# Optimization experiments

Hardware: AMD Instinct MI355X
Metric: run time of the kernel (lower is better)

Reference implementation:

```python
import jax, jax.numpy as jnp
import numpy as np

E = 2048        # embed_dim
HQ = 32         # num_query_heads
HKV = 8         # num_kv_heads
HD = E // HQ    # head_dim = 64
GROUP = HQ // HKV  # q_per_kv = 4
B, T = 2, 2048


def setup_inputs() -> dict:
    key = jax.random.key(0)
    ks = jax.random.split(key, 6)
    s = 0.02
    x  = jax.random.normal(ks[0], (B, T, E), dtype=jnp.float32)
    Wq = jax.random.normal(ks[1], (E, E), dtype=jnp.float32) * s
    Wk = jax.random.normal(ks[2], (E, HKV * HD), dtype=jnp.float32) * s
    Wv = jax.random.normal(ks[3], (E, HKV * HD), dtype=jnp.float32) * s
    Wo = jax.random.normal(ks[4], (E, E), dtype=jnp.float32) * s
    bo = jax.random.normal(ks[5], (E,), dtype=jnp.float32) * s
    return {"x": x, "Wq": Wq, "Wk": Wk, "Wv": Wv, "Wo": Wo, "bo": bo}


def reference(x, Wq, Wk, Wv, Wo, bo):
    Bc, Tc, _ = x.shape
    # projections
    q = (x @ Wq).reshape(Bc, Tc, HQ, HD).transpose(0, 2, 1, 3)      # [B,HQ,T,HD]
    k = (x @ Wk).reshape(Bc, Tc, HKV, HD).transpose(0, 2, 1, 3)     # [B,HKV,T,HD]
    v = (x @ Wv).reshape(Bc, Tc, HKV, HD).transpose(0, 2, 1, 3)     # [B,HKV,T,HD]
    # group queries by kv head instead of repeating k/v: [B,HKV,GROUP,T,HD]
    qg = q.reshape(Bc, HKV, GROUP, Tc, HD)
    scale = 1.0 / jnp.sqrt(jnp.asarray(HD, dtype=x.dtype))
    scores = jnp.einsum('bhgqd,bhkd->bhgqk', qg, k) * scale         # [B,HKV,GROUP,T,T]
    weights = jax.nn.softmax(scores, axis=-1)
    attn = jnp.einsum('bhgqk,bhkd->bhgqd', weights, v)              # [B,HKV,GROUP,T,HD]
    out = attn.reshape(Bc, HQ, Tc, HD).transpose(0, 2, 1, 3).reshape(Bc, Tc, E)
    return out @ Wo + bo
```

## Files before the change

### kernel.cpp

```cpp
#include <hip/hip_runtime.h>
#include <hip/hip_bf16.h>
#include <stdint.h>

#define E_ 2048
#define HQ_ 32
#define HKV_ 8
#define HD_ 64
#define B_ 2
#define T_ 2048
#define MROWS (B_*T_)
#define NKV (HKV_*HD_)
#define NQKV (E_ + 2*NKV)
#define SCALE_LOG2E 0.18033688011112042f

typedef __bf16 bf16_t;
typedef __bf16 bf16x8 __attribute__((ext_vector_type(8)));
typedef float f32x4 __attribute__((ext_vector_type(4)));

typedef const __attribute__((address_space(1))) unsigned int glb_u32;
typedef __attribute__((address_space(3))) unsigned int lds_u32;

__device__ __forceinline__ unsigned short f2bf_bits(float f) {
  unsigned int u = __float_as_uint(f);
  u += 0x7FFFu + ((u >> 16) & 1u);
  return (unsigned short)(u >> 16);
}
__device__ __forceinline__ bf16_t f2bf(float f) {
  union { unsigned short s; bf16_t h; } u;
  u.s = f2bf_bits(f);
  return u.h;
}

__global__ void cast_x_kernel(const float* __restrict__ in, bf16_t* __restrict__ out, int n8) {
  int i = blockIdx.x * blockDim.x + threadIdx.x;
  int stride = gridDim.x * blockDim.x;
  for (; i < n8; i += stride) {
    const float4* p = reinterpret_cast<const float4*>(in) + (size_t)i * 2;
    float4 a = p[0], b = p[1];
    union { unsigned short s[8]; uint4 v; } u;
    u.s[0] = f2bf_bits(a.x); u.s[1] = f2bf_bits(a.y);
    u.s[2] = f2bf_bits(a.z); u.s[3] = f2bf_bits(a.w);
    u.s[4] = f2bf_bits(b.x); u.s[5] = f2bf_bits(b.y);
    u.s[6] = f2bf_bits(b.z); u.s[7] = f2bf_bits(b.w);
    reinterpret_cast<uint4*>(out)[i] = u.v;
  }
}

__global__ void transpose_cast_w(const float* __restrict__ in, bf16_t* __restrict__ out,
                                 int R, int C) {
  __shared__ float tile[32][33];
  int c0 = blockIdx.x * 32, r0 = blockIdx.y * 32;
  int tx = threadIdx.x, ty = threadIdx.y;
#pragma unroll
  for (int j = 0; j < 4; ++j) {
    int r = ty + j * 8;
    tile[r][tx] = in[(size_t)(r0 + r) * C + c0 + tx];
  }
  __syncthreads();
#pragma unroll
  for (int j = 0; j < 4; ++j) {
    int c = ty + j * 8;
    out[(size_t)(c0 + c) * R + r0 + tx] = f2bf(tile[tx][c]);
  }
}

__global__ void transpose_v_kernel(const bf16_t* __restrict__ qkv, bf16_t* __restrict__ vt) {
  __shared__ bf16_t tile[32][33];
  int b = blockIdx.z;
  int hd0 = blockIdx.x * 32, t0 = blockIdx.y * 32;
  int tx = threadIdx.x, ty = threadIdx.y;
#pragma unroll
  for (int j = 0; j < 4; ++j) {
    int tt = ty + j * 8;
    tile[tt][tx] = qkv[(size_t)(b * T_ + t0 + tt) * NQKV + (E_ + NKV) + hd0 + tx];
  }
  __syncthreads();
#pragma unroll
  for (int j = 0; j < 4; ++j) {
    int hh = ty + j * 8;
    vt[(size_t)(b * NKV + hd0 + hh) * T_ + t0 + tx] = tile[tx][hh];
  }
}

template <int OUTMODE>
__global__ void gemm_bt_kernel(const bf16_t* __restrict__ A, const bf16_t* __restrict__ BT,
                               void* __restrict__ Cv, const float* __restrict__ bias,
                               int M, int N, int K) {
  __shared__ bf16_t As[128 * 32];
  __shared__ bf16_t Bs[128 * 32];
  int tid = threadIdx.x;
  int w = tid >> 6, lane = tid & 63;
  int l15 = lane & 15, l4 = lane >> 4;
  int m0 = blockIdx.x * 128, n0 = blockIdx.y * 128;
  int wm = (w >> 1) * 64, wn = (w & 1) * 64;

  f32x4 zero = {0.f, 0.f, 0.f, 0.f};
  f32x4 acc[4][4];
#pragma unroll
  for (int mt = 0; mt < 4; ++mt)
#pragma unroll
    for (int nt = 0; nt < 4; ++nt) acc[mt][nt] = zero;

  int nK = K >> 5;
  for (int kt = 0; kt < nK; ++kt) {
    int k0 = kt << 5;
#pragma unroll
    for (int j = 0; j < 2; ++j) {
      int c = w * 2 + j;
      int L = c * 512 + lane * 8;
      int row = L >> 5, col = L & 31;
      __builtin_amdgcn_global_load_lds((glb_u32*)(A + (size_t)(m0 + row) * K + k0 + col),
                                       (lds_u32*)(As + c * 512), 16, 0, 0);
      __builtin_amdgcn_global_load_lds((glb_u32*)(BT + (size_t)(n0 + row) * K + k0 + col),
                                       (lds_u32*)(Bs + c * 512), 16, 0, 0);
    }
    __syncthreads();

    bf16x8 afr[4], bfr[4];
#pragma unroll
    for (int t = 0; t < 4; ++t) {
      afr[t] = *reinterpret_cast<const bf16x8*>(As + (wm + t * 16 + l15) * 32 + l4 * 8);
      bfr[t] = *reinterpret_cast<const bf16x8*>(Bs + (wn + t * 16 + l15) * 32 + l4 * 8);
    }
#pragma unroll
    for (int mt = 0; mt < 4; ++mt)
#pragma unroll
      for (int nt = 0; nt < 4; ++nt)
        acc[mt][nt] = __builtin_amdgcn_mfma_f32_16x16x32_bf16(afr[mt], bfr[nt], acc[mt][nt], 0, 0, 0);
    __syncthreads();
  }

  if (OUTMODE == 0) {
    bf16_t* C = reinterpret_cast<bf16_t*>(Cv);
#pragma unroll
    for (int mt = 0; mt < 4; ++mt)
#pragma unroll
      for (int nt = 0; nt < 4; ++nt) {
        int n = n0 + wn + nt * 16 + l15;
#pragma unroll
        for (int r = 0; r < 4; ++r) {
          int m = m0 + wm + mt * 16 + l4 * 4 + r;
          C[(size_t)m * N + n] = f2bf(acc[mt][nt][r]);
        }
      }
  } else {
    float* C = reinterpret_cast<float*>(Cv);
#pragma unroll
    for (int mt = 0; mt < 4; ++mt)
#pragma unroll
      for (int nt = 0; nt < 4; ++nt) {
        int n = n0 + wn + nt * 16 + l15;
        float bb = bias[n];
#pragma unroll
        for (int r = 0; r < 4; ++r) {
          int m = m0 + wm + mt * 16 + l4 * 4 + r;
          C[(size_t)m * N + n] = acc[mt][nt][r] + bb;
        }
      }
  }
}

__global__ void attn_kernel(const bf16_t* __restrict__ qkv, const bf16_t* __restrict__ vt,
                            bf16_t* __restrict__ attn) {
  __shared__ bf16_t Kbuf[2][64 * 64];
  __shared__ bf16_t Vbuf[2][64 * 64];
  __shared__ bf16_t P_lds[8 * 16 * 72];

  int tid = threadIdx.x;
  int w = tid >> 6, lane = tid & 63;
  int l15 = lane & 15, l4 = lane >> 4;
  int bh = blockIdx.y;
  int b = bh >> 5, hq = bh & 31, hkv = hq >> 2;
  int q0 = blockIdx.x * 128 + w * 16;

  const bf16_t* qp = qkv + (size_t)(b * T_ + q0 + l15) * NQKV + hq * HD_ + l4 * 8;
  bf16x8 qf0 = *reinterpret_cast<const bf16x8*>(qp);
  bf16x8 qf1 = *reinterpret_cast<const bf16x8*>(qp + 32);

  f32x4 zero = {0.f, 0.f, 0.f, 0.f};
  f32x4 o[4];
  float m_i[4], l_i[4];
#pragma unroll
  for (int dt = 0; dt < 4; ++dt) o[dt] = zero;
#pragma unroll
  for (int r = 0; r < 4; ++r) { m_i[r] = -1e30f; l_i[r] = 0.f; }

  bf16_t* Pw = P_lds + w * 16 * 72;

  int srow = w * 8 + (lane >> 3);
  int schunk = (lane & 7) ^ ((lane >> 3) & 7);
  const bf16_t* kg = qkv + (size_t)b * T_ * NQKV + E_ + hkv * HD_;
  const bf16_t* vg = vt + ((size_t)(b * HKV_ + hkv) * HD_ + srow) * T_;

#define STAGE_KV(bi, kv0) do {                                                          \
    __builtin_amdgcn_global_load_lds(                                                   \
        (glb_u32*)(kg + (size_t)((kv0) + srow) * NQKV + schunk * 8),                    \
        (lds_u32*)(&Kbuf[bi][w * 8 * 64]), 16, 0, 0);                                   \
    __builtin_amdgcn_global_load_lds(                                                   \
        (glb_u32*)(vg + (kv0) + schunk * 8),                                            \
        (lds_u32*)(&Vbuf[bi][w * 8 * 64]), 16, 0, 0);                                   \
  } while (0)

  STAGE_KV(0, 0);
  __syncthreads();

#pragma unroll 2
  for (int t = 0; t < T_ / 64; ++t) {
    int bi = t & 1;
    if (t < T_ / 64 - 1) STAGE_KV(bi ^ 1, (t + 1) * 64);

    f32x4 s[4];
    __builtin_amdgcn_s_setprio(1);
#pragma unroll
    for (int j = 0; j < 4; ++j) {
      int kr = j * 16 + l15;
      const bf16_t* kb = &Kbuf[bi][kr * 64];
      bf16x8 kf0 = *reinterpret_cast<const bf16x8*>(kb + ((l4 ^ (kr & 7)) * 8));
      bf16x8 kf1 = *reinterpret_cast<const bf16x8*>(kb + (((4 + l4) ^ (kr & 7)) * 8));
      f32x4 z = zero;
      z = __builtin_amdgcn_mfma_f32_16x16x32_bf16(qf0, kf0, z, 0, 0, 0);
      z = __builtin_amdgcn_mfma_f32_16x16x32_bf16(qf1, kf1, z, 0, 0, 0);
      s[j] = z;
    }
    __builtin_amdgcn_s_setprio(0);

    float p[4][4];
#pragma unroll
    for (int r = 0; r < 4; ++r) {
      float v = fmaxf(fmaxf(s[0][r], s[1][r]), fmaxf(s[2][r], s[3][r]));
#pragma unroll
      for (int off = 1; off < 16; off <<= 1) v = fmaxf(v, __shfl_xor(v, off));
      float mnew = fmaxf(m_i[r], v);
      float corr = exp2f((m_i[r] - mnew) * SCALE_LOG2E);
      l_i[r] *= corr;
#pragma unroll
      for (int dt = 0; dt < 4; ++dt) o[dt][r] *= corr;
      m_i[r] = mnew;
      float ssum = 0.f;
#pragma unroll
      for (int j = 0; j < 4; ++j) {
        p[j][r] = exp2f((s[j][r] - mnew) * SCALE_LOG2E);
        ssum += p[j][r];
      }
#pragma unroll
      for (int off = 1; off < 16; off <<= 1) ssum += __shfl_xor(ssum, off);
      l_i[r] += ssum;
    }

#pragma unroll
    for (int j = 0; j < 4; ++j)
#pragma unroll
      for (int r = 0; r < 4; ++r)
        Pw[(l4 * 4 + r) * 72 + j * 16 + l15] = f2bf(p[j][r]);
    asm volatile("s_waitcnt lgkmcnt(0)" ::: "memory");
    bf16x8 pf0 = *reinterpret_cast<const bf16x8*>(Pw + l15 * 72 + l4 * 8);
    bf16x8 pf1 = *reinterpret_cast<const bf16x8*>(Pw + l15 * 72 + l4 * 8 + 32);

    __builtin_amdgcn_s_setprio(1);
#pragma unroll
    for (int dt = 0; dt < 4; ++dt) {
      int vr = dt * 16 + l15;
      const bf16_t* vb = &Vbuf[bi][vr * 64];
      bf16x8 vf0 = *reinterpret_cast<const bf16x8*>(vb + ((l4 ^ (vr & 7)) * 8));
      bf16x8 vf1 = *reinterpret_cast<const bf16x8*>(vb + (((4 + l4) ^ (vr & 7)) * 8));
      o[dt] = __builtin_amdgcn_mfma_f32_16x16x32_bf16(pf0, vf0, o[dt], 0, 0, 0);
      o[dt] = __builtin_amdgcn_mfma_f32_16x16x32_bf16(pf1, vf1, o[dt], 0, 0, 0);
    }
    __builtin_amdgcn_s_setprio(0);

    __syncthreads();
  }
#undef STAGE_KV

  float rl[4];
#pragma unroll
  for (int r = 0; r < 4; ++r) rl[r] = 1.0f / l_i[r];
#pragma unroll
  for (int dt = 0; dt < 4; ++dt)
#pragma unroll
    for (int r = 0; r < 4; ++r)
      attn[(size_t)(b * T_ + q0 + l4 * 4 + r) * E_ + hq * HD_ + dt * 16 + l15] =
          f2bf(o[dt][r] * rl[r]);
}

extern "C" void kernel_launch(void* const* d_in, const int* in_sizes, int n_in,
                              void* d_out, int out_size, void* d_ws, size_t ws_size,
                              hipStream_t stream) {
  const float* x  = (const float*)d_in[0];
  const float* Wq = (const float*)d_in[1];
  const float* Wk = (const float*)d_in[2];
  const float* Wv = (const float*)d_in[3];
  const float* Wo = (const float*)d_in[4];
  const float* bo = (const float*)d_in[5];
  float* out = (float*)d_out;

  bf16_t* xb    = (bf16_t*)d_ws;
  bf16_t* WcatT = xb + (size_t)MROWS * E_;
  bf16_t* WoT   = WcatT + (size_t)NQKV * E_;
  bf16_t* QKV   = WoT + (size_t)E_ * E_;
  bf16_t* Vt    = QKV + (size_t)MROWS * NQKV;
  bf16_t* Attn  = Vt + (size_t)B_ * NKV * T_;

  dim3 tblk(32, 8);
  cast_x_kernel<<<2048, 256, 0, stream>>>(x, xb, MROWS * E_ / 8);
  transpose_cast_w<<<dim3(E_ / 32, E_ / 32), tblk, 0, stream>>>(Wq, WcatT, E_, E_);
  transpose_cast_w<<<dim3(NKV / 32, E_ / 32), tblk, 0, stream>>>(Wk, WcatT + (size_t)E_ * E_, E_, NKV);
  transpose_cast_w<<<dim3(NKV / 32, E_ / 32), tblk, 0, stream>>>(Wv, WcatT + (size_t)(E_ + NKV) * E_, E_, NKV);
  transpose_cast_w<<<dim3(E_ / 32, E_ / 32), tblk, 0, stream>>>(Wo, WoT, E_, E_);

  gemm_bt_kernel<0><<<dim3(MROWS / 128, NQKV / 128), 256, 0, stream>>>(
      xb, WcatT, (void*)QKV, nullptr, MROWS, NQKV, E_);

  transpose_v_kernel<<<dim3(NKV / 32, T_ / 32, B_), tblk, 0, stream>>>(QKV, Vt);

  attn_kernel<<<dim3(T_ / 128, B_ * HQ_), 512, 0, stream>>>(QKV, Vt, Attn);

  gemm_bt_kernel<1><<<dim3(MROWS / 128, E_ / 128), 256, 0, stream>>>(
      Attn, WoT, (void*)out, bo, MROWS, E_, E_);
}
```

Before: 430.8 us.

## Rewrite attention with 32x32 MFMA, transposed scores, lazy rescale, register P

The attention kernel moves from 16x16x32 to 32x32x16 bf16 MFMA, with each wave handling 32 query rows and computing S^T so each lane owns one query column. The P matrix is handed to the PV MFMA through cross-half lane shuffles instead of an LDS round trip. The softmax scale is folded into Q, exp2 uses the hardware builtin, and the running max is rescaled only when it grows by more than 8. This halves the attention grid to 256 queries per block, cutting softmax reductions and LDS traffic, at the cost of more registers, fewer blocks and extra bf16 rounding of scaled Q.

Result: faster. 381.8 us (-11.4%).

```diff
diff --git a/kernel.cpp b/kernel.cpp
--- a/kernel.cpp
+++ b/kernel.cpp
@@ -16,6 +16,7 @@
 typedef __bf16 bf16_t;
 typedef __bf16 bf16x8 __attribute__((ext_vector_type(8)));
 typedef float f32x4 __attribute__((ext_vector_type(4)));
+typedef float f32x16 __attribute__((ext_vector_type(16)));
 
 typedef const __attribute__((address_space(1))) unsigned int glb_u32;
 typedef __attribute__((address_space(3))) unsigned int lds_u32;
@@ -29,6 +30,18 @@
   union { unsigned short s; bf16_t h; } u;
   u.s = f2bf_bits(f);
   return u.h;
+}
+__device__ __forceinline__ unsigned pack2bf(float lo, float hi) {
+  union { struct { bf16_t l, h; } s; unsigned u; } c;
+  c.s.l = (bf16_t)lo; c.s.h = (bf16_t)hi;
+  return c.u;
+}
+__device__ __forceinline__ float fexp2(float x) {
+#if __has_builtin(__builtin_amdgcn_exp2f)
+  return __builtin_amdgcn_exp2f(x);
+#else
+  return exp2f(x);
+#endif
 }
 
 __global__ void cast_x_kernel(const float* __restrict__ in, bf16_t* __restrict__ out, int n8) {
@@ -164,28 +177,30 @@
                             bf16_t* __restrict__ attn) {
   __shared__ bf16_t Kbuf[2][64 * 64];
   __shared__ bf16_t Vbuf[2][64 * 64];
-  __shared__ bf16_t P_lds[8 * 16 * 72];
+  __shared__ float bcast[8][32];
 
   int tid = threadIdx.x;
   int w = tid >> 6, lane = tid & 63;
-  int l15 = lane & 15, l4 = lane >> 4;
+  int l31 = lane & 31, hi = lane >> 5;
   int bh = blockIdx.y;
   int b = bh >> 5, hq = bh & 31, hkv = hq >> 2;
-  int q0 = blockIdx.x * 128 + w * 16;
-
-  const bf16_t* qp = qkv + (size_t)(b * T_ + q0 + l15) * NQKV + hq * HD_ + l4 * 8;
-  bf16x8 qf0 = *reinterpret_cast<const bf16x8*>(qp);
-  bf16x8 qf1 = *reinterpret_cast<const bf16x8*>(qp + 32);
-
-  f32x4 zero = {0.f, 0.f, 0.f, 0.f};
-  f32x4 o[4];
-  float m_i[4], l_i[4];
-#pragma unroll
-  for (int dt = 0; dt < 4; ++dt) o[dt] = zero;
-#pragma unroll
-  for (int r = 0; r < 4; ++r) { m_i[r] = -1e30f; l_i[r] = 0.f; }
-
-  bf16_t* Pw = P_lds + w * 16 * 72;
+  int q0 = blockIdx.x * 256 + w * 32;
+
+  bf16x8 qf[4];
+  {
+    const bf16_t* qp = qkv + (size_t)(b * T_ + q0 + l31) * NQKV + hq * HD_;
+#pragma unroll
+    for (int s = 0; s < 4; ++s) {
+      bf16x8 q = *reinterpret_cast<const bf16x8*>(qp + s * 16 + hi * 8);
+#pragma unroll
+      for (int e = 0; e < 8; ++e) q[e] = (bf16_t)((float)q[e] * SCALE_LOG2E);
+      qf[s] = q;
+    }
+  }
+
+  f32x16 o0 = {0.f,0.f,0.f,0.f,0.f,0.f,0.f,0.f,0.f,0.f,0.f,0.f,0.f,0.f,0.f,0.f};
+  f32x16 o1 = o0;
+  float m_r = -1e30f, l_r = 0.f;
 
   int srow = w * 8 + (lane >> 3);
   int schunk = (lane & 7) ^ ((lane >> 3) & 7);
@@ -201,6 +216,13 @@
         (lds_u32*)(&Vbuf[bi][w * 8 * 64]), 16, 0, 0);                                   \
   } while (0)
 
+#define KREAD(bi, tsub, s) \
+  (*reinterpret_cast<const bf16x8*>(&Kbuf[bi][((tsub) * 32 + l31) * 64 + \
+      ((((s) * 2 + hi) ^ (l31 & 7)) * 8)]))
+#define VREAD(bi, dh, s) \
+  (*reinterpret_cast<const bf16x8*>(&Vbuf[bi][((dh) * 32 + l31) * 64 + \
+      ((((s) * 2 + hi) ^ (l31 & 7)) * 8)]))
+
   STAGE_KV(0, 0);
   __syncthreads();
 
@@ -209,78 +231,90 @@
     int bi = t & 1;
     if (t < T_ / 64 - 1) STAGE_KV(bi ^ 1, (t + 1) * 64);
 
-    f32x4 s[4];
+    f32x16 sa = {0.f,0.f,0.f,0.f,0.f,0.f,0.f,0.f,0.f,0.f,0.f,0.f,0.f,0.f,0.f,0.f};
+    f32x16 sb = sa;
     __builtin_amdgcn_s_setprio(1);
 #pragma unroll
-    for (int j = 0; j < 4; ++j) {
-      int kr = j * 16 + l15;
-      const bf16_t* kb = &Kbuf[bi][kr * 64];
-      bf16x8 kf0 = *reinterpret_cast<const bf16x8*>(kb + ((l4 ^ (kr & 7)) * 8));
-      bf16x8 kf1 = *reinterpret_cast<const bf16x8*>(kb + (((4 + l4) ^ (kr & 7)) * 8));
-      f32x4 z = zero;
-      z = __builtin_amdgcn_mfma_f32_16x16x32_bf16(qf0, kf0, z, 0, 0, 0);
-      z = __builtin_amdgcn_mfma_f32_16x16x32_bf16(qf1, kf1, z, 0, 0, 0);
-      s[j] = z;
+    for (int s = 0; s < 4; ++s) {
+      sa = __builtin_amdgcn_mfma_f32_32x32x16_bf16(KREAD(bi, 0, s), qf[s], sa, 0, 0, 0);
+      sb = __builtin_amdgcn_mfma_f32_32x32x16_bf16(KREAD(bi, 1, s), qf[s], sb, 0, 0, 0);
     }
     __builtin_amdgcn_s_setprio(0);
 
-    float p[4][4];
-#pragma unroll
-    for (int r = 0; r < 4; ++r) {
-      float v = fmaxf(fmaxf(s[0][r], s[1][r]), fmaxf(s[2][r], s[3][r]));
-#pragma unroll
-      for (int off = 1; off < 16; off <<= 1) v = fmaxf(v, __shfl_xor(v, off));
-      float mnew = fmaxf(m_i[r], v);
-      float corr = exp2f((m_i[r] - mnew) * SCALE_LOG2E);
-      l_i[r] *= corr;
-#pragma unroll
-      for (int dt = 0; dt < 4; ++dt) o[dt][r] *= corr;
-      m_i[r] = mnew;
-      float ssum = 0.f;
-#pragma unroll
-      for (int j = 0; j < 4; ++j) {
-        p[j][r] = exp2f((s[j][r] - mnew) * SCALE_LOG2E);
-        ssum += p[j][r];
+    float pmax = sa[0];
+#pragma unroll
+    for (int r = 1; r < 16; ++r) pmax = fmaxf(pmax, sa[r]);
+#pragma unroll
+    for (int r = 0; r < 16; ++r) pmax = fmaxf(pmax, sb[r]);
+
+    if (__any(pmax > m_r + 8.f)) {
+      float pm2 = __shfl_xor(pmax, 32);
+      float mnew = fmaxf(m_r, fmaxf(pmax, pm2));
+      float corr = fexp2(m_r - mnew);
+      m_r = mnew;
+      l_r *= corr;
+      bcast[w][l31] = corr;
+      asm volatile("s_waitcnt lgkmcnt(0)" ::: "memory");
+#pragma unroll
+      for (int r = 0; r < 16; ++r) {
+        float c = bcast[w][(r & 3) + 8 * (r >> 2) + 4 * hi];
+        o0[r] *= c; o1[r] *= c;
       }
-#pragma unroll
-      for (int off = 1; off < 16; off <<= 1) ssum += __shfl_xor(ssum, off);
-      l_i[r] += ssum;
-    }
-
-#pragma unroll
-    for (int j = 0; j < 4; ++j)
-#pragma unroll
-      for (int r = 0; r < 4; ++r)
-        Pw[(l4 * 4 + r) * 72 + j * 16 + l15] = f2bf(p[j][r]);
-    asm volatile("s_waitcnt lgkmcnt(0)" ::: "memory");
-    bf16x8 pf0 = *reinterpret_cast<const bf16x8*>(Pw + l15 * 72 + l4 * 8);
-    bf16x8 pf1 = *reinterpret_cast<const bf16x8*>(Pw + l15 * 72 + l4 * 8 + 32);
+    }
+
+    float pA[16], pB[16];
+    float ps0 = 0.f, ps1 = 0.f;
+#pragma unroll
+    for (int r = 0; r < 16; ++r) {
+      pA[r] = fexp2(sa[r] - m_r); ps0 += pA[r];
+      pB[r] = fexp2(sb[r] - m_r); ps1 += pB[r];
+    }
+    l_r += ps0 + ps1;
+
+    unsigned wd[2][4][2];
+#pragma unroll
+    for (int g = 0; g < 4; ++g)
+#pragma unroll
+      for (int j = 0; j < 2; ++j) {
+        wd[0][g][j] = pack2bf(pA[4 * g + 2 * j], pA[4 * g + 2 * j + 1]);
+        wd[1][g][j] = pack2bf(pB[4 * g + 2 * j], pB[4 * g + 2 * j + 1]);
+      }
 
     __builtin_amdgcn_s_setprio(1);
 #pragma unroll
-    for (int dt = 0; dt < 4; ++dt) {
-      int vr = dt * 16 + l15;
-      const bf16_t* vb = &Vbuf[bi][vr * 64];
-      bf16x8 vf0 = *reinterpret_cast<const bf16x8*>(vb + ((l4 ^ (vr & 7)) * 8));
-      bf16x8 vf1 = *reinterpret_cast<const bf16x8*>(vb + (((4 + l4) ^ (vr & 7)) * 8));
-      o[dt] = __builtin_amdgcn_mfma_f32_16x16x32_bf16(pf0, vf0, o[dt], 0, 0, 0);
-      o[dt] = __builtin_amdgcn_mfma_f32_16x16x32_bf16(pf1, vf1, o[dt], 0, 0, 0);
+    for (int s = 0; s < 4; ++s) {
+      const int tt = s >> 1, gg = 2 * (s & 1);
+      unsigned send0 = hi ? wd[tt][gg][0] : wd[tt][gg + 1][0];
+      unsigned send1 = hi ? wd[tt][gg][1] : wd[tt][gg + 1][1];
+      unsigned recv0 = __shfl_xor(send0, 32);
+      unsigned recv1 = __shfl_xor(send1, 32);
+      union { unsigned u[4]; bf16x8 v; } pf;
+      pf.u[0] = hi ? recv0 : wd[tt][gg][0];
+      pf.u[1] = hi ? recv1 : wd[tt][gg][1];
+      pf.u[2] = hi ? wd[tt][gg + 1][0] : recv0;
+      pf.u[3] = hi ? wd[tt][gg + 1][1] : recv1;
+      o0 = __builtin_amdgcn_mfma_f32_32x32x16_bf16(pf.v, VREAD(bi, 0, s), o0, 0, 0, 0);
+      o1 = __builtin_amdgcn_mfma_f32_32x32x16_bf16(pf.v, VREAD(bi, 1, s), o1, 0, 0, 0);
     }
     __builtin_amdgcn_s_setprio(0);
 
     __syncthreads();
   }
 #undef STAGE_KV
-
-  float rl[4];
-#pragma unroll
-  for (int r = 0; r < 4; ++r) rl[r] = 1.0f / l_i[r];
-#pragma unroll
-  for (int dt = 0; dt < 4; ++dt)
-#pragma unroll
-    for (int r = 0; r < 4; ++r)
-      attn[(size_t)(b * T_ + q0 + l4 * 4 + r) * E_ + hq * HD_ + dt * 16 + l15] =
-          f2bf(o[dt][r] * rl[r]);
+#undef KREAD
+#undef VREAD
+
+  float lfull = l_r + __shfl_xor(l_r, 32);
+  bcast[w][l31] = 1.0f / lfull;
+  asm volatile("s_waitcnt lgkmcnt(0)" ::: "memory");
+  const size_t obase = (size_t)(b * T_ + q0) * E_ + hq * HD_;
+#pragma unroll
+  for (int r = 0; r < 16; ++r) {
+    int q = (r & 3) + 8 * (r >> 2) + 4 * hi;
+    float rl = bcast[w][q];
+    attn[obase + (size_t)q * E_ + l31]      = (bf16_t)(o0[r] * rl);
+    attn[obase + (size_t)q * E_ + 32 + l31] = (bf16_t)(o1[r] * rl);
+  }
 }
 
 extern "C" void kernel_launch(void* const* d_in, const int* in_sizes, int n_in,
@@ -313,7 +347,7 @@
 
   transpose_v_kernel<<<dim3(NKV / 32, T_ / 32, B_), tblk, 0, stream>>>(QKV, Vt);
 
-  attn_kernel<<<dim3(T_ / 128, B_ * HQ_), 512, 0, stream>>>(QKV, Vt, Attn);
+  attn_kernel<<<dim3(T_ / 256, B_ * HQ_), 512, 0, stream>>>(QKV, Vt, Attn);
 
   gemm_bt_kernel<1><<<dim3(MROWS / 128, E_ / 128), 256, 0, stream>>>(
       Attn, WoT, (void*)out, bo, MROWS, E_, E_);
```
